# Performance work log

Hardware: AMD Instinct MI355X
Metric: run time of the kernel (lower is better)

The kernel has to match this reference:

```python
import jax, jax.numpy as jnp
import numpy as np

EPS = 1e-6
CONV_P = 3.0
GM_P = 2.0
NUM_NODES = 50000
NUM_EDGES = 600000
NUM_GRAPHS = 512
IN_DIM = 128
HID = 128
OUT_DIM = 64


def _scatter_mean(vals, index, num_segments):
    # scatter_mean with empty segments -> 0 (count clamped to 1)
    s = jax.ops.segment_sum(vals, index, num_segments=num_segments)
    cnt = jax.ops.segment_sum(jnp.ones((vals.shape[0],), vals.dtype), index,
                              num_segments=num_segments)
    return s / jnp.maximum(cnt, 1.0)[:, None]


def _signed_pow(v, p):
    return jnp.sign(v) * (jnp.abs(v) + EPS) ** p


def _spm_conv(x, W, b, src, dst, p):
    h = x @ W.T + b                      # [N, hid] linear
    msg = h[src]                          # gather x_j  [E, hid]
    t = _signed_pow(msg, p)
    pooled = _scatter_mean(t, dst, NUM_NODES)
    return _signed_pow(pooled, 1.0 / p)


def setup_inputs() -> dict:
    key = jax.random.key(0)
    ks = jax.random.split(key, 8)
    x = jax.random.normal(ks[0], (NUM_NODES, IN_DIM), jnp.float32)
    edge_index = jax.random.randint(ks[1], (2, NUM_EDGES), 0, NUM_NODES)
    batch = jnp.sort(jax.random.randint(ks[2], (NUM_NODES,), 0, NUM_GRAPHS))
    s1 = 1.0 / np.sqrt(IN_DIM)
    s2 = 1.0 / np.sqrt(HID)
    W1 = jax.random.uniform(ks[3], (HID, IN_DIM), jnp.float32, -s1, s1)
    b1 = jax.random.uniform(ks[4], (HID,), jnp.float32, -s1, s1)
    W2 = jax.random.uniform(ks[5], (HID, HID), jnp.float32, -s2, s2)
    b2 = jax.random.uniform(ks[6], (HID,), jnp.float32, -s2, s2)
    # final layer: orthogonal-init frozen weight (out_dim=64, hid=128)
    A = jax.random.normal(ks[7], (HID, OUT_DIM), jnp.float32)
    Q, _ = jnp.linalg.qr(A)
    Wout = Q.T                            # [OUT_DIM, HID], orthonormal rows
    bout = jax.random.uniform(jax.random.fold_in(key, 9), (OUT_DIM,),
                              jnp.float32, -s2, s2)
    return {"x": x, "W1": W1, "b1": b1, "W2": W2, "b2": b2,
            "Wout": Wout, "bout": bout, "edge_index": edge_index,
            "batch": batch}


def reference(x, W1, b1, W2, b2, Wout, bout, edge_index, batch):
    src, dst = edge_index[0], edge_index[1]
    h = _spm_conv(x, W1, b1, src, dst, CONV_P)
    h = jax.nn.relu(h)                    # relu between conv layers only
    h = _spm_conv(h, W2, b2, src, dst, CONV_P)
    # global generalized mean pool (signed)
    t = _signed_pow(h, GM_P)
    pooled = _scatter_mean(t, batch, NUM_GRAPHS)
    graph_repr = _signed_pow(pooled, 1.0 / GM_P)   # [G, HID]
    return graph_repr @ Wout.T + bout              # [G, OUT_DIM]
```

## Files before the change

### kernel.cpp

```cpp
#include <hip/hip_runtime.h>
#include <hip/hip_bf16.h>
#include <math.h>

#define N_NODES 50000
#define N_EDGES 600000
#define N_GRAPHS 512
#define DIM 128
#define OUTD 64
#define EPSV 1e-6f
#define BSTRIDE 64
#define EBLK 2344

typedef __attribute__((ext_vector_type(8))) short bf16x8;
typedef __attribute__((ext_vector_type(4))) float f32x4;

__device__ __forceinline__ float sgn(float v) {
    return (v > 0.f) ? 1.f : ((v < 0.f) ? -1.f : 0.f);
}

__device__ __forceinline__ float cube_signed(float v) {
    float m = fabsf(v) + EPSV;
    return sgn(v) * m * m * m;
}

__device__ __forceinline__ float cbrt_pos(float m) {
    return exp2f(log2f(m) * (1.0f / 3.0f));
}

__device__ __forceinline__ unsigned short f2bf(float f) {
    unsigned u = __float_as_uint(f);
    unsigned r = (u + 0x7fff + ((u >> 16) & 1)) >> 16;
    return (unsigned short)r;
}

__device__ __forceinline__ float bf2f(unsigned short h) {
    return __uint_as_float(((unsigned)h) << 16);
}

__device__ __forceinline__ void gather_acc8(const unsigned* __restrict__ T32,
                                            const unsigned short* __restrict__ bucket,
                                            int cnt, int lane, float2 acc[4]) {
    #pragma unroll
    for (int j = 0; j < 4; j++) acc[j] = make_float2(0.f, 0.f);
    if (cnt <= 0) return;
    int myidx = (lane < cnt) ? (int)bucket[lane] : 0;
    int sub = lane & 15, grp = lane >> 4;
    int cnt16 = (cnt + 15) & ~15;
    for (int i = 0; i < cnt16; i += 16) {
        uint4 u[4];
        #pragma unroll
        for (int c = 0; c < 4; c++) {
            int s = __shfl(myidx, i + c * 4 + grp, 64);
            u[c] = *(const uint4*)(T32 + (size_t)s * 64 + sub * 4);
        }
        #pragma unroll
        for (int c = 0; c < 4; c++) {
            acc[0].x += __uint_as_float(u[c].x << 16);
            acc[0].y += __uint_as_float(u[c].x & 0xffff0000u);
            acc[1].x += __uint_as_float(u[c].y << 16);
            acc[1].y += __uint_as_float(u[c].y & 0xffff0000u);
            acc[2].x += __uint_as_float(u[c].z << 16);
            acc[2].y += __uint_as_float(u[c].z & 0xffff0000u);
            acc[3].x += __uint_as_float(u[c].w << 16);
            acc[3].y += __uint_as_float(u[c].w & 0xffff0000u);
        }
    }
    #pragma unroll
    for (int j = 0; j < 4; j++) {
        acc[j].x += __shfl_xor(acc[j].x, 16, 64);
        acc[j].y += __shfl_xor(acc[j].y, 16, 64);
        acc[j].x += __shfl_xor(acc[j].x, 32, 64);
        acc[j].y += __shfl_xor(acc[j].y, 32, 64);
    }
}

__device__ __forceinline__ float acc_pick_x(const float2 acc[4], int grp) {
    return grp == 0 ? acc[0].x : grp == 1 ? acc[1].x : grp == 2 ? acc[2].x : acc[3].x;
}
__device__ __forceinline__ float acc_pick_y(const float2 acc[4], int grp) {
    return grp == 0 ? acc[0].y : grp == 1 ? acc[1].y : grp == 2 ? acc[2].y : acc[3].y;
}


__global__ void prep(const float* __restrict__ W1, const float* __restrict__ W2,
                     unsigned short* __restrict__ W1hi, unsigned short* __restrict__ W1lo,
                     unsigned short* __restrict__ W2hi, unsigned short* __restrict__ W2lo,
                     int* __restrict__ deg,
                     const int* __restrict__ batch, int* __restrict__ gstart,
                     unsigned* __restrict__ T1z, unsigned* __restrict__ T2z) {
    int i = blockIdx.x * 256 + threadIdx.x;
    {
        float w = W1[i];
        unsigned short h = f2bf(w);
        W1hi[i] = h;
        W1lo[i] = f2bf(w - bf2f(h));
        w = W2[i];
        h = f2bf(w);
        W2hi[i] = h;
        W2lo[i] = f2bf(w - bf2f(h));
    }
    if (i < 64) { T1z[i] = 0u; T2z[i] = 0u; }
    if (i <= N_GRAPHS) {
        int lo = 0, hi = N_NODES;
        while (lo < hi) {
            int mid = (lo + hi) >> 1;
            if (batch[mid] < i) lo = mid + 1; else hi = mid;
        }
        gstart[i] = lo;
    }
    for (int j = i; j < N_NODES; j += 16384) deg[j] = 0;
}


__global__ void build(const int* __restrict__ src, const int* __restrict__ dst,
                      int* __restrict__ deg, unsigned short* __restrict__ csr) {
    int e = blockIdx.x * 256 + threadIdx.x;
    if (e < N_EDGES) {
        int d = dst[e];
        int slot = atomicAdd(&deg[d], 1);
        if (slot < BSTRIDE) csr[d * BSTRIDE + slot] = (unsigned short)(src[e] + 1);
    }
}


__global__ __launch_bounds__(256) void linear_cube_mfma(const float* __restrict__ X,
                                                        const unsigned short* __restrict__ Whi,
                                                        const unsigned short* __restrict__ Wlo,
                                                        const float* __restrict__ B,
                                                        unsigned short* __restrict__ T) {
    int wave = threadIdx.x >> 6;
    int lane = threadIdx.x & 63;
    int tile = blockIdx.x * 4 + wave;
    if (tile >= N_NODES / 16) return;
    int n0 = tile * 16;
    int r = lane & 15;
    int g = lane >> 4;

    bf16x8 xh[4], xl[4];
    const float* xrow = X + (size_t)(n0 + r) * DIM + g * 8;
    #pragma unroll
    for (int kb = 0; kb < 4; kb++) {
        float4 a = *(const float4*)(xrow + kb * 32);
        float4 b = *(const float4*)(xrow + kb * 32 + 4);
        float v[8] = {a.x, a.y, a.z, a.w, b.x, b.y, b.z, b.w};
        #pragma unroll
        for (int j = 0; j < 8; j++) {
            unsigned short h = f2bf(v[j]);
            float rem = v[j] - bf2f(h);
            xh[kb][j] = (short)h;
            xl[kb][j] = (short)f2bf(rem);
        }
    }

    #pragma unroll
    for (int ct = 0; ct < 8; ct++) {
        const unsigned short* whbase = Whi + (size_t)(ct * 16 + r) * DIM + g * 8;
        const unsigned short* wlbase = Wlo + (size_t)(ct * 16 + r) * DIM + g * 8;
        f32x4 acc = {0.f, 0.f, 0.f, 0.f};
        #pragma unroll
        for (int kb = 0; kb < 4; kb++) {
            bf16x8 wh = *(const bf16x8*)(whbase + kb * 32);
            bf16x8 wl = *(const bf16x8*)(wlbase + kb * 32);
            acc = __builtin_amdgcn_mfma_f32_16x16x32_bf16(xh[kb], wh, acc, 0, 0, 0);
            acc = __builtin_amdgcn_mfma_f32_16x16x32_bf16(xl[kb], wh, acc, 0, 0, 0);
            acc = __builtin_amdgcn_mfma_f32_16x16x32_bf16(xh[kb], wl, acc, 0, 0, 0);
        }
        float bias = B[ct * 16 + r];
        #pragma unroll
        for (int q = 0; q < 4; q++) {
            int node = g * 4 + q;
            float h = acc[q] + bias;
            T[(size_t)(n0 + node + 1) * DIM + ct * 16 + r] = f2bf(cube_signed(h));
        }
    }
}


__global__ __launch_bounds__(512) void agg_linear_cube(const unsigned* __restrict__ T32,
                                                       const int* __restrict__ deg,
                                                       const unsigned short* __restrict__ csr,
                                                       const unsigned short* __restrict__ Whi,
                                                       const unsigned short* __restrict__ Wlo,
                                                       const float* __restrict__ B,
                                                       unsigned short* __restrict__ Tout) {
    __shared__ __attribute__((aligned(16))) unsigned Phi[16][68];
    __shared__ __attribute__((aligned(16))) unsigned Plo[16][68];
    int wave = threadIdx.x >> 6;
    int lane = threadIdx.x & 63;
    int n0 = blockIdx.x * 16;
    int sub = lane & 15, grp = lane >> 4;

    #pragma unroll
    for (int q = 0; q < 2; q++) {
        int row = wave * 2 + q;
        int nd = n0 + row;
        int d = deg[nd];
        int cnt = d < BSTRIDE ? d : BSTRIDE;
        float2 acc[4];
        gather_acc8(T32, csr + (size_t)nd * BSTRIDE, cnt, lane, acc);
        float c = (float)(d > 1 ? d : 1);
        float m0 = acc_pick_x(acc, grp) / c;
        float m1 = acc_pick_y(acc, grp) / c;
        float r0 = fmaxf(sgn(m0) * cbrt_pos(fabsf(m0) + EPSV), 0.f);
        float r1 = fmaxf(sgn(m1) * cbrt_pos(fabsf(m1) + EPSV), 0.f);
        unsigned short h0 = f2bf(r0), h1 = f2bf(r1);
        unsigned short l0 = f2bf(r0 - bf2f(h0)), l1 = f2bf(r1 - bf2f(h1));
        Phi[row][sub * 4 + grp] = (unsigned)h0 | ((unsigned)h1 << 16);
        Plo[row][sub * 4 + grp] = (unsigned)l0 | ((unsigned)l1 << 16);
    }
    __syncthreads();

    int r = lane & 15;
    int g = lane >> 4;
    bf16x8 xh[4], xl[4];
    #pragma unroll
    for (int kb = 0; kb < 4; kb++) {
        xh[kb] = *(const bf16x8*)&Phi[r][kb * 16 + g * 4];
        xl[kb] = *(const bf16x8*)&Plo[r][kb * 16 + g * 4];
    }
    int ct = wave;
    const unsigned short* whbase = Whi + (size_t)(ct * 16 + r) * DIM + g * 8;
    const unsigned short* wlbase = Wlo + (size_t)(ct * 16 + r) * DIM + g * 8;
    f32x4 acc = {0.f, 0.f, 0.f, 0.f};
    #pragma unroll
    for (int kb = 0; kb < 4; kb++) {
        bf16x8 wh = *(const bf16x8*)(whbase + kb * 32);
        bf16x8 wl = *(const bf16x8*)(wlbase + kb * 32);
        acc = __builtin_amdgcn_mfma_f32_16x16x32_bf16(xh[kb], wh, acc, 0, 0, 0);
        acc = __builtin_amdgcn_mfma_f32_16x16x32_bf16(xl[kb], wh, acc, 0, 0, 0);
        acc = __builtin_amdgcn_mfma_f32_16x16x32_bf16(xh[kb], wl, acc, 0, 0, 0);
    }
    float bias = B[ct * 16 + r];
    #pragma unroll
    for (int q = 0; q < 4; q++) {
        int node = g * 4 + q;
        float h = acc[q] + bias;
        Tout[(size_t)(n0 + node + 1) * DIM + ct * 16 + r] = f2bf(cube_signed(h));
    }
}


__global__ __launch_bounds__(256) void aggregate(const unsigned* __restrict__ T32,
                                                 const int* __restrict__ deg,
                                                 const unsigned short* __restrict__ csr,
                                                 float* __restrict__ P) {
    int nd = blockIdx.x * 4 + (threadIdx.x >> 6);
    if (nd >= N_NODES) return;
    int lane = threadIdx.x & 63;
    int sub = lane & 15, grp = lane >> 4;
    int d = deg[nd];
    int cnt = d < BSTRIDE ? d : BSTRIDE;
    float2 acc[4];
    gather_acc8(T32, csr + (size_t)nd * BSTRIDE, cnt, lane, acc);
    float c = (float)(d > 1 ? d : 1);
    float m0 = acc_pick_x(acc, grp) / c;
    float m1 = acc_pick_y(acc, grp) / c;
    float r0 = sgn(m0) * cbrt_pos(fabsf(m0) + EPSV);
    float r1 = sgn(m1) * cbrt_pos(fabsf(m1) + EPSV);
    *(float2*)(P + (size_t)nd * DIM + sub * 8 + grp * 2) = make_float2(r0, r1);
}


__global__ __launch_bounds__(128) void pool_final(const float* __restrict__ P,
                                                  const int* __restrict__ gstart,
                                                  const float* __restrict__ Wout,
                                                  const float* __restrict__ bout,
                                                  float* __restrict__ out) {
    __shared__ float R[DIM];
    __shared__ float partial[128];
    int g = blockIdx.x, f = threadIdx.x;
    int s = gstart[g], e = gstart[g + 1];
    float acc = 0.f;
    for (int i = s; i < e; i++) {
        float v = P[(size_t)i * DIM + f];
        float m = fabsf(v) + EPSV;
        acc += sgn(v) * m * m;
    }
    int cnt = e - s;
    float c = (float)(cnt > 1 ? cnt : 1);
    float mean = acc / c;
    R[f] = sgn(mean) * sqrtf(fabsf(mean) + EPSV);
    __syncthreads();

    int o = f & 63;
    int half = f >> 6;
    const float4* W4 = (const float4*)Wout + o * 32 + half * 16;
    const float4* R4 = (const float4*)R + half * 16;
    float a = 0.f;
    #pragma unroll
    for (int k = 0; k < 16; k++) {
        float4 w = W4[k];
        float4 r = R4[k];
        a += r.x * w.x + r.y * w.y + r.z * w.z + r.w * w.w;
    }
    partial[f] = a;
    __syncthreads();
    if (f < OUTD) out[(size_t)g * OUTD + f] = bout[f] + partial[f] + partial[f + 64];
}


extern "C" void kernel_launch(void* const* d_in, const int* in_sizes, int n_in,
                              void* d_out, int out_size, void* d_ws, size_t ws_size,
                              hipStream_t stream) {
    const float* x    = (const float*)d_in[0];
    const float* W1   = (const float*)d_in[1];
    const float* b1   = (const float*)d_in[2];
    const float* W2   = (const float*)d_in[3];
    const float* b2   = (const float*)d_in[4];
    const float* Wout = (const float*)d_in[5];
    const float* bout = (const float*)d_in[6];
    const int* edge   = (const int*)d_in[7];
    const int* batch  = (const int*)d_in[8];
    const int* srcp = edge;
    const int* dstp = edge + N_EDGES;
    float* out = (float*)d_out;

    char* ws = (char*)d_ws;
    size_t off = 0;
    auto alloc = [&](size_t bytes) -> char* {
        char* p = ws + off;
        off += (bytes + 255) / 256 * 256;
        return p;
    };
    unsigned short* T1 = (unsigned short*)alloc((size_t)(N_NODES + 1) * DIM * 2);
    unsigned short* T2 = (unsigned short*)alloc((size_t)(N_NODES + 1) * DIM * 2);
    float* P        = (float*)alloc((size_t)N_NODES * DIM * 4);
    int*   deg      = (int*)alloc((size_t)N_NODES * 4);
    unsigned short* csr = (unsigned short*)alloc((size_t)N_NODES * BSTRIDE * 2);
    int*   gstart   = (int*)alloc((size_t)(N_GRAPHS + 1) * 4);
    unsigned short* W1hi = (unsigned short*)alloc((size_t)DIM * DIM * 2);
    unsigned short* W1lo = (unsigned short*)alloc((size_t)DIM * DIM * 2);
    unsigned short* W2hi = (unsigned short*)alloc((size_t)DIM * DIM * 2);
    unsigned short* W2lo = (unsigned short*)alloc((size_t)DIM * DIM * 2);

    prep<<<64, 256, 0, stream>>>(W1, W2, W1hi, W1lo, W2hi, W2lo,
                                 deg, batch, gstart,
                                 (unsigned*)T1, (unsigned*)T2);
    build<<<EBLK, 256, 0, stream>>>(srcp, dstp, deg, csr);

    const int TILES = N_NODES / 16;
    const int LBLK = (TILES + 3) / 4;
    const int ABLK = (N_NODES + 3) / 4;
    linear_cube_mfma<<<LBLK, 256, 0, stream>>>(x, W1hi, W1lo, b1, T1);
    agg_linear_cube<<<TILES, 512, 0, stream>>>((const unsigned*)T1, deg, csr,
                                               W2hi, W2lo, b2, T2);
    aggregate<<<ABLK, 256, 0, stream>>>((const unsigned*)T2, deg, csr, P);
    pool_final<<<N_GRAPHS, 128, 0, stream>>>(P, gstart, Wout, bout, out);
}
```

Before: 186.3 us.

## Fuse prep and CSR build into one kernel, vectorize edges, stage outputs in LDS

Merges the weight-split/gstart prep kernel with the CSR build kernel into one launch. Degree zeroing moves to a hipMemsetAsync, and each build thread now handles four edges using uint4 loads. The first linear kernel writes its bf16 cube outputs into shared memory per wave and then stores whole rows to global memory with coalesced uint4 writes, replacing the strided 2-byte stores. This cuts launch count and improves store coalescing, at the cost of an extra memset call and more shared memory per block.

```diff
diff --git a/kernel.cpp b/kernel.cpp
--- a/kernel.cpp
+++ b/kernel.cpp
@@ -9,7 +9,8 @@
 #define OUTD 64
 #define EPSV 1e-6f
 #define BSTRIDE 64
-#define EBLK 2344
+#define EBLK4 586
+#define PREP_BLK 64
 
 typedef __attribute__((ext_vector_type(8))) short bf16x8;
 typedef __attribute__((ext_vector_type(4))) float f32x4;
@@ -82,13 +83,32 @@
 }
 
 
-__global__ void prep(const float* __restrict__ W1, const float* __restrict__ W2,
-                     unsigned short* __restrict__ W1hi, unsigned short* __restrict__ W1lo,
-                     unsigned short* __restrict__ W2hi, unsigned short* __restrict__ W2lo,
-                     int* __restrict__ deg,
-                     const int* __restrict__ batch, int* __restrict__ gstart,
-                     unsigned* __restrict__ T1z, unsigned* __restrict__ T2z) {
-    int i = blockIdx.x * 256 + threadIdx.x;
+__global__ void buildprep(const int* __restrict__ src, const int* __restrict__ dst,
+                          int* __restrict__ deg, unsigned short* __restrict__ csr,
+                          const float* __restrict__ W1, const float* __restrict__ W2,
+                          unsigned short* __restrict__ W1hi, unsigned short* __restrict__ W1lo,
+                          unsigned short* __restrict__ W2hi, unsigned short* __restrict__ W2lo,
+                          const int* __restrict__ batch, int* __restrict__ gstart,
+                          unsigned* __restrict__ T1z, unsigned* __restrict__ T2z) {
+    int b = blockIdx.x;
+    if (b < EBLK4) {
+        int e4 = b * 256 + threadIdx.x;
+        if (e4 < N_EDGES / 4) {
+            uint4 s4 = ((const uint4*)src)[e4];
+            uint4 d4 = ((const uint4*)dst)[e4];
+            int d0 = (int)d4.x, d1 = (int)d4.y, d2 = (int)d4.z, d3 = (int)d4.w;
+            int sl0 = atomicAdd(&deg[d0], 1);
+            int sl1 = atomicAdd(&deg[d1], 1);
+            int sl2 = atomicAdd(&deg[d2], 1);
+            int sl3 = atomicAdd(&deg[d3], 1);
+            if (sl0 < BSTRIDE) csr[d0 * BSTRIDE + sl0] = (unsigned short)(s4.x + 1);
+            if (sl1 < BSTRIDE) csr[d1 * BSTRIDE + sl1] = (unsigned short)(s4.y + 1);
+            if (sl2 < BSTRIDE) csr[d2 * BSTRIDE + sl2] = (unsigned short)(s4.z + 1);
+            if (sl3 < BSTRIDE) csr[d3 * BSTRIDE + sl3] = (unsigned short)(s4.w + 1);
+        }
+        return;
+    }
+    int i = (b - EBLK4) * 256 + threadIdx.x;
     {
         float w = W1[i];
         unsigned short h = f2bf(w);
@@ -108,18 +128,6 @@
         }
         gstart[i] = lo;
     }
-    for (int j = i; j < N_NODES; j += 16384) deg[j] = 0;
-}
-
-
-__global__ void build(const int* __restrict__ src, const int* __restrict__ dst,
-                      int* __restrict__ deg, unsigned short* __restrict__ csr) {
-    int e = blockIdx.x * 256 + threadIdx.x;
-    if (e < N_EDGES) {
-        int d = dst[e];
-        int slot = atomicAdd(&deg[d], 1);
-        if (slot < BSTRIDE) csr[d * BSTRIDE + slot] = (unsigned short)(src[e] + 1);
-    }
 }
 
 
@@ -128,6 +136,7 @@
                                                         const unsigned short* __restrict__ Wlo,
                                                         const float* __restrict__ B,
                                                         unsigned short* __restrict__ T) {
+    __shared__ unsigned short Tl[4][16][DIM];
     int wave = threadIdx.x >> 6;
     int lane = threadIdx.x & 63;
     int tile = blockIdx.x * 4 + wave;
@@ -170,8 +179,15 @@
         for (int q = 0; q < 4; q++) {
             int node = g * 4 + q;
             float h = acc[q] + bias;
-            T[(size_t)(n0 + node + 1) * DIM + ct * 16 + r] = f2bf(cube_signed(h));
-        }
+            Tl[wave][node][ct * 16 + r] = f2bf(cube_signed(h));
+        }
+    }
+
+    uint4* dstg = (uint4*)(T + (size_t)(n0 + 1) * DIM);
+    const uint4* srcl = (const uint4*)&Tl[wave][0][0];
+    #pragma unroll
+    for (int i = 0; i < 4; i++) {
+        dstg[i * 64 + lane] = srcl[i * 64 + lane];
     }
 }
 
@@ -333,10 +349,11 @@
     unsigned short* W2hi = (unsigned short*)alloc((size_t)DIM * DIM * 2);
     unsigned short* W2lo = (unsigned short*)alloc((size_t)DIM * DIM * 2);
 
-    prep<<<64, 256, 0, stream>>>(W1, W2, W1hi, W1lo, W2hi, W2lo,
-                                 deg, batch, gstart,
-                                 (unsigned*)T1, (unsigned*)T2);
-    build<<<EBLK, 256, 0, stream>>>(srcp, dstp, deg, csr);
+    hipMemsetAsync(deg, 0, (size_t)N_NODES * 4, stream);
+    buildprep<<<EBLK4 + PREP_BLK, 256, 0, stream>>>(srcp, dstp, deg, csr,
+                                                    W1, W2, W1hi, W1lo, W2hi, W2lo,
+                                                    batch, gstart,
+                                                    (unsigned*)T1, (unsigned*)T2);
 
     const int TILES = N_NODES / 16;
     const int LBLK = (TILES + 3) / 4;
```

Result: no change. 182.9 us, median of 2 (-1.8%).
